# Kernel tuning notes

Measured on AMD Instinct MI355X. Metric: run time of the kernel, lower is better.

The kernel has to match this reference:

```python
import jax, jax.numpy as jnp
import numpy as np

N_NODES = 100000
N_EDGES = 1000000
IN_DIM = 128
HID1 = 64
HID2 = 64
OUT_DIM = 1
NUM_GRAPHS = 2048


def setup_inputs() -> dict:
    key = jax.random.key(0)
    ks = jax.random.split(key, 12)
    x = jax.random.normal(ks[0], (N_NODES, IN_DIM), dtype=jnp.float32)
    edge_index = jax.random.randint(ks[1], (2, N_EDGES), 0, N_NODES, dtype=jnp.int64)
    batch = jnp.sort(jax.random.randint(ks[2], (N_NODES,), 0, NUM_GRAPHS, dtype=jnp.int64))
    s1 = 1.0 / np.sqrt(IN_DIM)
    s2 = 1.0 / np.sqrt(HID1)
    s3 = 1.0 / np.sqrt(HID2)
    return {
        "x": x,
        "edge_index": edge_index,
        "batch": batch,
        "W1": jax.random.normal(ks[3], (IN_DIM, HID1), dtype=jnp.float32) * s1,
        "b1": jnp.zeros((HID1,), dtype=jnp.float32),
        "W2": jax.random.normal(ks[4], (HID1, HID2), dtype=jnp.float32) * s2,
        "b2": jnp.zeros((HID2,), dtype=jnp.float32),
        "attn_w": jax.random.normal(ks[5], (HID2, 1), dtype=jnp.float32) * s3,
        "attn_b": jnp.zeros((1,), dtype=jnp.float32),
        "mask_w": jax.random.normal(ks[6], (HID2, 1), dtype=jnp.float32) * s3,
        "mask_b": jnp.zeros((1,), dtype=jnp.float32),
        "out_w": jax.random.normal(ks[7], (HID2, OUT_DIM), dtype=jnp.float32) * s3,
        "out_b": jnp.zeros((OUT_DIM,), dtype=jnp.float32),
    }


def reference(x, edge_index, batch, W1, b1, W2, b2, attn_w, attn_b, mask_w, mask_b, out_w, out_b):
    n = x.shape[0]
    # GCNConv (PyG default): add self-loops, symmetric normalization
    loop = jnp.arange(n, dtype=edge_index.dtype)
    row = jnp.concatenate([edge_index[0], loop])  # source nodes
    col = jnp.concatenate([edge_index[1], loop])  # target nodes
    deg = jax.ops.segment_sum(jnp.ones_like(col, dtype=x.dtype), col, num_segments=n)
    dinv = jnp.where(deg > 0, jax.lax.rsqrt(jnp.maximum(deg, 1e-12)), 0.0)
    norm = dinv[row] * dinv[col]  # [E+N]

    def conv(h, W, b):
        h = h @ W                              # [N, out]
        m = h[row] * norm[:, None]             # gather + scale  [E+N, out]
        return jax.ops.segment_sum(m, col, num_segments=n) + b

    h = jax.nn.relu(conv(x, W1, b1))
    h = jax.nn.relu(conv(h, W2, b2))
    # AttentionPooling: (attn score * sigmoid mask)-weighted scatter-sum per graph
    scores = (h @ attn_w + attn_b) * jax.nn.sigmoid(h @ mask_w + mask_b)  # [N,1]
    pooled = jax.ops.segment_sum(h * scores, batch, num_segments=NUM_GRAPHS)  # [G, HID2]
    return pooled @ out_w + out_b
```

## Files before the change

kernel.cpp:

```cpp
#include <hip/hip_runtime.h>
#include <math.h>


#define NB 64
#define SEG 16
#define CAPS 80
#define SLOTS (SEG * CAPS)
#define BIN_BLOCKS 256

__global__ __launch_bounds__(256) void gemm_bin_kernel(
    const float* __restrict__ X, const float* __restrict__ W,
    float* __restrict__ P, int N, int K,
    const int* __restrict__ row, const int* __restrict__ col,
    int* __restrict__ bcnt, int* __restrict__ gbuf, int E,
    float* __restrict__ out, const float* __restrict__ out_b, int G) {
    __shared__ float Wl[32 * 64];
    __shared__ float xs[128 * 33];

    if (blockIdx.x < BIN_BLOCKS) {
        int seg = blockIdx.x & (SEG - 1);
        int t = blockIdx.x * 256 + threadIdx.x;
        if (t < G) out[t] = out_b[0];
        for (int e = t; e < E; e += BIN_BLOCKS * 256) {
            int c = col[e];
            int b = c >> 6;
            int pos = atomicAdd(&bcnt[(b * SEG + seg) * 16], 1);
            if (pos < CAPS) gbuf[b * SLOTS + seg * CAPS + pos] = row[e] | ((c & 63) << 17);
        }
        return;
    }

    const int tid = threadIdx.x;
    const int cg = tid & 3;
    const int ng = tid >> 2;
    const int node0 = (blockIdx.x - BIN_BLOCKS) * 128;

    float acc[2][16];
#pragma unroll
    for (int r = 0; r < 2; r++)
#pragma unroll
        for (int j = 0; j < 16; j++) acc[r][j] = 0.0f;

    for (int k0 = 0; k0 < K; k0 += 32) {
        const float4* Wg = (const float4*)(W + (size_t)k0 * 64);
#pragma unroll
        for (int f = tid; f < 512; f += 256) ((float4*)Wl)[f] = Wg[f];
        {
            int rrow = tid >> 1;
            int q0 = (tid & 1) * 16;
            int node = node0 + rrow;
            const float* Xr = X + (size_t)node * K + k0 + q0;
            float* xd = &xs[rrow * 33 + q0];
#pragma unroll
            for (int q = 0; q < 4; q++) {
                float4 v = make_float4(0.f, 0.f, 0.f, 0.f);
                if (node < N) v = *(const float4*)(Xr + 4 * q);
                xd[4 * q + 0] = v.x;
                xd[4 * q + 1] = v.y;
                xd[4 * q + 2] = v.z;
                xd[4 * q + 3] = v.w;
            }
        }
        __syncthreads();
#pragma unroll
        for (int kk = 0; kk < 32; kk++) {
            float xv0 = xs[(ng * 2 + 0) * 33 + kk];
            float xv1 = xs[(ng * 2 + 1) * 33 + kk];
            const float* wr = &Wl[kk * 64 + cg * 4];
            float4 w0 = *(const float4*)(wr + 0);
            float4 w1 = *(const float4*)(wr + 16);
            float4 w2 = *(const float4*)(wr + 32);
            float4 w3 = *(const float4*)(wr + 48);
#pragma unroll
            for (int r = 0; r < 2; r++) {
                float xv = r ? xv1 : xv0;
                acc[r][0]  = fmaf(xv, w0.x, acc[r][0]);
                acc[r][1]  = fmaf(xv, w0.y, acc[r][1]);
                acc[r][2]  = fmaf(xv, w0.z, acc[r][2]);
                acc[r][3]  = fmaf(xv, w0.w, acc[r][3]);
                acc[r][4]  = fmaf(xv, w1.x, acc[r][4]);
                acc[r][5]  = fmaf(xv, w1.y, acc[r][5]);
                acc[r][6]  = fmaf(xv, w1.z, acc[r][6]);
                acc[r][7]  = fmaf(xv, w1.w, acc[r][7]);
                acc[r][8]  = fmaf(xv, w2.x, acc[r][8]);
                acc[r][9]  = fmaf(xv, w2.y, acc[r][9]);
                acc[r][10] = fmaf(xv, w2.z, acc[r][10]);
                acc[r][11] = fmaf(xv, w2.w, acc[r][11]);
                acc[r][12] = fmaf(xv, w3.x, acc[r][12]);
                acc[r][13] = fmaf(xv, w3.y, acc[r][13]);
                acc[r][14] = fmaf(xv, w3.z, acc[r][14]);
                acc[r][15] = fmaf(xv, w3.w, acc[r][15]);
            }
        }
        __syncthreads();
    }

#pragma unroll
    for (int r = 0; r < 2; r++) {
        int node = node0 + ng * 2 + r;
        if (node < N) {
            float* dst = P + (size_t)node * 64 + cg * 4;
#pragma unroll
            for (int m = 0; m < 4; m++) {
                float4 v = make_float4(acc[r][4 * m + 0], acc[r][4 * m + 1],
                                       acc[r][4 * m + 2], acc[r][4 * m + 3]);
                *(float4*)(dst + 16 * m) = v;
            }
        }
    }
}

__global__ __launch_bounds__(256) void sort_scale_kernel(
    const int* __restrict__ bcnt, const int* __restrict__ gbuf,
    int* __restrict__ csr, int* __restrict__ startcnt,
    float* __restrict__ dinv, float* __restrict__ P, int N) {
    __shared__ int scnt[SEG], segoff[SEG], s_tot;
    __shared__ int ebuf[SLOTS];
    __shared__ int lcnt[NB], lstart[NB], lcur[NB];
    __shared__ float dinv_s[NB];
    const int tid = threadIdx.x;
    const int b = blockIdx.x;
    const int base = b * SLOTS;

    if (tid < SEG) {
        int c = bcnt[(b * SEG + tid) * 16];
        scnt[tid] = c < CAPS ? c : CAPS;
    }
    if (tid < NB) lcnt[tid] = 0;
    __syncthreads();
    if (tid == 0) {
        int o = 0;
        for (int s = 0; s < SEG; s++) { segoff[s] = o; o += scnt[s]; }
        s_tot = o;
    }
    __syncthreads();
    for (int idx = tid; idx < SLOTS; idx += 256) {
        int seg = idx / CAPS;
        int j = idx - seg * CAPS;
        if (j < scnt[seg]) {
            int w = gbuf[base + idx];
            ebuf[segoff[seg] + j] = w;
            atomicAdd(&lcnt[(w >> 17) & 63], 1);
        }
    }
    __syncthreads();
    if (tid < NB) {
        int cntv = lcnt[tid];
        int val = cntv;
#pragma unroll
        for (int off = 1; off < 64; off <<= 1) {
            int n = __shfl_up(val, off, 64);
            if (tid >= off) val += n;
        }
        int st = val - cntv;
        lstart[tid] = st;
        lcur[tid] = st;
        float dv = rsqrtf(1.0f + (float)cntv);
        dinv_s[tid] = dv;
        int v = b * NB + tid;
        if (v < N) {
            dinv[v] = dv;
            int cc = cntv < 127 ? cntv : 127;
            startcnt[v] = ((base + st) << 7) | cc;
        }
    }
    __syncthreads();
    int tot = s_tot;
    for (int idx = tid; idx < tot; idx += 256) {
        int w = ebuf[idx];
        int vl = (w >> 17) & 63;
        int pp = atomicAdd(&lcur[vl], 1);
        csr[base + pp] = w & 131071;
    }
    const int g = tid >> 4;
    const int p4 = (tid & 15) * 4;
    for (int s = 0; s < 4; s++) {
        int vl = g + s * 16;
        int v = b * NB + vl;
        if (v < N) {
            float d = dinv_s[vl];
            float4 x = *(const float4*)(P + (size_t)v * 64 + p4);
            x.x *= d; x.y *= d; x.z *= d; x.w *= d;
            *(float4*)(P + (size_t)v * 64 + p4) = x;
        }
    }
}

__global__ __launch_bounds__(256) void gather_kernel(
    const float* __restrict__ P, const int* __restrict__ csr,
    const int* __restrict__ startcnt, const float* __restrict__ dinv,
    const float* __restrict__ bias, float* __restrict__ B, int N) {
    int t = blockIdx.x * blockDim.x + threadIdx.x;
    int v = t >> 4;
    if (v >= N) return;
    int p4 = (t & 15) * 4;
    int pack = startcnt[v];
    int st = pack >> 7;
    int c = pack & 127;
    float dv = dinv[v];
    float4 acc = *(const float4*)(P + (size_t)v * 64 + p4);
    for (int i = 0; i < c; i += 4) {
        int i1 = (i + 1 < c) ? i + 1 : i;
        int i2 = (i + 2 < c) ? i + 2 : i;
        int i3 = (i + 3 < c) ? i + 3 : i;
        int u0 = csr[st + i], u1 = csr[st + i1], u2 = csr[st + i2], u3 = csr[st + i3];
        float4 m0 = *(const float4*)(P + (size_t)u0 * 64 + p4);
        float4 m1 = *(const float4*)(P + (size_t)u1 * 64 + p4);
        float4 m2 = *(const float4*)(P + (size_t)u2 * 64 + p4);
        float4 m3 = *(const float4*)(P + (size_t)u3 * 64 + p4);
        acc.x += m0.x; acc.y += m0.y; acc.z += m0.z; acc.w += m0.w;
        if (i + 1 < c) { acc.x += m1.x; acc.y += m1.y; acc.z += m1.z; acc.w += m1.w; }
        if (i + 2 < c) { acc.x += m2.x; acc.y += m2.y; acc.z += m2.z; acc.w += m2.w; }
        if (i + 3 < c) { acc.x += m3.x; acc.y += m3.y; acc.z += m3.z; acc.w += m3.w; }
    }
    float4 bb = *(const float4*)(bias + p4);
    float4 r;
    r.x = fmaxf(fmaf(acc.x, dv, bb.x), 0.f);
    r.y = fmaxf(fmaf(acc.y, dv, bb.y), 0.f);
    r.z = fmaxf(fmaf(acc.z, dv, bb.z), 0.f);
    r.w = fmaxf(fmaf(acc.w, dv, bb.w), 0.f);
    *(float4*)(B + (size_t)v * 64 + p4) = r;
}

__global__ __launch_bounds__(256) void gemm_scale_kernel(
    const float* __restrict__ X, const float* __restrict__ W,
    const float* __restrict__ dinv, float* __restrict__ Q, int N, int K) {
    __shared__ float Wl[32 * 64];
    __shared__ float xs[128 * 33];
    const int tid = threadIdx.x;
    const int cg = tid & 3;
    const int ng = tid >> 2;
    const int node0 = blockIdx.x * 128;

    float acc[2][16];
#pragma unroll
    for (int r = 0; r < 2; r++)
#pragma unroll
        for (int j = 0; j < 16; j++) acc[r][j] = 0.0f;

    for (int k0 = 0; k0 < K; k0 += 32) {
        const float4* Wg = (const float4*)(W + (size_t)k0 * 64);
#pragma unroll
        for (int f = tid; f < 512; f += 256) ((float4*)Wl)[f] = Wg[f];
        {
            int rrow = tid >> 1;
            int q0 = (tid & 1) * 16;
            int node = node0 + rrow;
            const float* Xr = X + (size_t)node * K + k0 + q0;
            float* xd = &xs[rrow * 33 + q0];
#pragma unroll
            for (int q = 0; q < 4; q++) {
                float4 v = make_float4(0.f, 0.f, 0.f, 0.f);
                if (node < N) v = *(const float4*)(Xr + 4 * q);
                xd[4 * q + 0] = v.x;
                xd[4 * q + 1] = v.y;
                xd[4 * q + 2] = v.z;
                xd[4 * q + 3] = v.w;
            }
        }
        __syncthreads();
#pragma unroll
        for (int kk = 0; kk < 32; kk++) {
            float xv0 = xs[(ng * 2 + 0) * 33 + kk];
            float xv1 = xs[(ng * 2 + 1) * 33 + kk];
            const float* wr = &Wl[kk * 64 + cg * 4];
            float4 w0 = *(const float4*)(wr + 0);
            float4 w1 = *(const float4*)(wr + 16);
            float4 w2 = *(const float4*)(wr + 32);
            float4 w3 = *(const float4*)(wr + 48);
#pragma unroll
            for (int r = 0; r < 2; r++) {
                float xv = r ? xv1 : xv0;
                acc[r][0]  = fmaf(xv, w0.x, acc[r][0]);
                acc[r][1]  = fmaf(xv, w0.y, acc[r][1]);
                acc[r][2]  = fmaf(xv, w0.z, acc[r][2]);
                acc[r][3]  = fmaf(xv, w0.w, acc[r][3]);
                acc[r][4]  = fmaf(xv, w1.x, acc[r][4]);
                acc[r][5]  = fmaf(xv, w1.y, acc[r][5]);
                acc[r][6]  = fmaf(xv, w1.z, acc[r][6]);
                acc[r][7]  = fmaf(xv, w1.w, acc[r][7]);
                acc[r][8]  = fmaf(xv, w2.x, acc[r][8]);
                acc[r][9]  = fmaf(xv, w2.y, acc[r][9]);
                acc[r][10] = fmaf(xv, w2.z, acc[r][10]);
                acc[r][11] = fmaf(xv, w2.w, acc[r][11]);
                acc[r][12] = fmaf(xv, w3.x, acc[r][12]);
                acc[r][13] = fmaf(xv, w3.y, acc[r][13]);
                acc[r][14] = fmaf(xv, w3.z, acc[r][14]);
                acc[r][15] = fmaf(xv, w3.w, acc[r][15]);
            }
        }
        __syncthreads();
    }

#pragma unroll
    for (int r = 0; r < 2; r++) {
        int node = node0 + ng * 2 + r;
        if (node < N) {
            float d = dinv[node];
            float* dst = Q + (size_t)node * 64 + cg * 4;
#pragma unroll
            for (int m = 0; m < 4; m++) {
                float4 v = make_float4(acc[r][4 * m + 0] * d, acc[r][4 * m + 1] * d,
                                       acc[r][4 * m + 2] * d, acc[r][4 * m + 3] * d);
                *(float4*)(dst + 16 * m) = v;
            }
        }
    }
}

#define GP_NODES 64
__global__ __launch_bounds__(256) void gather_pool_kernel(
    const float* __restrict__ Q, const int* __restrict__ csr,
    const int* __restrict__ startcnt, const float* __restrict__ dinv,
    const float* __restrict__ bias, const int* __restrict__ batch,
    const float* __restrict__ attn_w, const float* __restrict__ attn_b,
    const float* __restrict__ mask_w, const float* __restrict__ mask_b,
    const float* __restrict__ out_w, float* __restrict__ out, int N) {
    __shared__ float pacc[2048];
    __shared__ int s_gmin, s_span;
    const int tid = threadIdx.x;
    const int v0 = blockIdx.x * GP_NODES;
    const int vend = (v0 + GP_NODES < N) ? v0 + GP_NODES : N;
    if (tid == 0) {
        int gmin = batch[v0];
        s_gmin = gmin;
        s_span = batch[vend - 1] - gmin + 1;
    }
    __syncthreads();
    const int gmin = s_gmin, span = s_span;
    for (int i = tid; i < span; i += 256) pacc[i] = 0.f;
    __syncthreads();

    const int p = tid & 15;
    const int p4 = p * 4;
    const float4 wa = ((const float4*)attn_w)[p];
    const float4 wm = ((const float4*)mask_w)[p];
    const float4 wo = ((const float4*)out_w)[p];
    const float4 bb = ((const float4*)bias)[p];
    const float ab = attn_b[0], mb = mask_b[0];

    for (int v = v0 + (tid >> 4); v < vend; v += 16) {
        int pack = startcnt[v];
        int st = pack >> 7;
        int c = pack & 127;
        float dv = dinv[v];
        float4 acc = *(const float4*)(Q + (size_t)v * 64 + p4);
        for (int i = 0; i < c; i += 4) {
            int i1 = (i + 1 < c) ? i + 1 : i;
            int i2 = (i + 2 < c) ? i + 2 : i;
            int i3 = (i + 3 < c) ? i + 3 : i;
            int u0 = csr[st + i], u1 = csr[st + i1], u2 = csr[st + i2], u3 = csr[st + i3];
            float4 m0 = *(const float4*)(Q + (size_t)u0 * 64 + p4);
            float4 m1 = *(const float4*)(Q + (size_t)u1 * 64 + p4);
            float4 m2 = *(const float4*)(Q + (size_t)u2 * 64 + p4);
            float4 m3 = *(const float4*)(Q + (size_t)u3 * 64 + p4);
            acc.x += m0.x; acc.y += m0.y; acc.z += m0.z; acc.w += m0.w;
            if (i + 1 < c) { acc.x += m1.x; acc.y += m1.y; acc.z += m1.z; acc.w += m1.w; }
            if (i + 2 < c) { acc.x += m2.x; acc.y += m2.y; acc.z += m2.z; acc.w += m2.w; }
            if (i + 3 < c) { acc.x += m3.x; acc.y += m3.y; acc.z += m3.z; acc.w += m3.w; }
        }
        float hx = fmaxf(fmaf(acc.x, dv, bb.x), 0.f);
        float hy = fmaxf(fmaf(acc.y, dv, bb.y), 0.f);
        float hz = fmaxf(fmaf(acc.z, dv, bb.z), 0.f);
        float hw = fmaxf(fmaf(acc.w, dv, bb.w), 0.f);
        float pa = hx * wa.x + hy * wa.y + hz * wa.z + hw * wa.w;
        float pm = hx * wm.x + hy * wm.y + hz * wm.z + hw * wm.w;
        float po = hx * wo.x + hy * wo.y + hz * wo.z + hw * wo.w;
#pragma unroll
        for (int off = 1; off < 16; off <<= 1) {
            pa += __shfl_xor(pa, off, 64);
            pm += __shfl_xor(pm, off, 64);
            po += __shfl_xor(po, off, 64);
        }
        if (p == 0) {
            float cc = (pa + ab) * (1.0f / (1.0f + expf(-(pm + mb)))) * po;
            atomicAdd(&pacc[batch[v] - gmin], cc);
        }
    }
    __syncthreads();
    for (int i = tid; i < span; i += 256) {
        float val = pacc[i];
        if (val != 0.f) atomicAdd(&out[gmin + i], val);
    }
}

extern "C" void kernel_launch(void* const* d_in, const int* in_sizes, int n_in,
                              void* d_out, int out_size, void* d_ws, size_t ws_size,
                              hipStream_t stream) {
    const float* x      = (const float*)d_in[0];
    const int*   edge   = (const int*)d_in[1];
    const int*   batch  = (const int*)d_in[2];
    const float* W1     = (const float*)d_in[3];
    const float* b1     = (const float*)d_in[4];
    const float* W2     = (const float*)d_in[5];
    const float* b2     = (const float*)d_in[6];
    const float* attn_w = (const float*)d_in[7];
    const float* attn_b = (const float*)d_in[8];
    const float* mask_w = (const float*)d_in[9];
    const float* mask_b = (const float*)d_in[10];
    const float* out_w  = (const float*)d_in[11];
    const float* out_b  = (const float*)d_in[12];
    float* out = (float*)d_out;

    const int N  = in_sizes[2];
    const int E  = in_sizes[1] / 2;
    const int K1 = in_sizes[0] / N;
    const int H  = in_sizes[4];
    const int G  = out_size;
    const int* row = edge;
    const int* col = edge + E;

    const int NBUCK = (N + NB - 1) / NB;

    char* ws = (char*)d_ws;
    auto align256 = [](size_t s) { return (s + 255) / 256 * 256; };
    int*   bcnt     = (int*)ws;   ws += align256((size_t)NBUCK * SEG * 16 * 4);
    int*   gbuf     = (int*)ws;   ws += align256((size_t)NBUCK * SLOTS * 4);
    int*   csr      = (int*)ws;   ws += align256((size_t)NBUCK * SLOTS * 4);
    int*   startcnt = (int*)ws;   ws += align256((size_t)N * 4);
    float* dinv     = (float*)ws; ws += align256((size_t)N * 4);
    float* P        = (float*)ws; ws += align256((size_t)N * H * 4);
    float* B        = (float*)ws; ws += align256((size_t)N * H * 4);
    float* Q        = (float*)ws;

    const int gblocks = (N + 127) / 128;
    const int n16b = (N * 16 + 255) / 256;

    hipMemsetAsync(bcnt, 0, (size_t)NBUCK * SEG * 16 * 4, stream);

    gemm_bin_kernel<<<BIN_BLOCKS + gblocks, 256, 0, stream>>>(
        x, W1, P, N, K1, row, col, bcnt, gbuf, E, out, out_b, G);

    sort_scale_kernel<<<NBUCK, 256, 0, stream>>>(
        bcnt, gbuf, csr, startcnt, dinv, P, N);

    gather_kernel<<<n16b, 256, 0, stream>>>(P, csr, startcnt, dinv, b1, B, N);

    gemm_scale_kernel<<<gblocks, 256, 0, stream>>>(B, W2, dinv, Q, N, H);

    gather_pool_kernel<<<NBUCK, 256, 0, stream>>>(
        Q, csr, startcnt, dinv, b2, batch, attn_w, attn_b, mask_w, mask_b, out_w, out, N);
}
```

Measured before the change: 277.0 us.

## Drop P prescale pass, pad CSR rows to 4 and vectorize neighbor index loads

The sort kernel no longer rescales P by dinv. The first gather instead multiplies each neighbor row by that neighbor's dinv, fetched separately, which removes a full read-modify-write pass over P. CSR segments are padded to multiples of 4 and zeroed by a new memset, so both gather loops can load neighbor indices as int4 and process 8 neighbors per iteration. The cost is an extra memset of the CSR buffer and an extra dinv gather per edge in layer one. Padding also consumes more of the fixed per-bucket slots, which could overflow a bucket's capacity.

```diff
diff --git a/kernel.cpp b/kernel.cpp
--- a/kernel.cpp
+++ b/kernel.cpp
@@ -110,14 +110,13 @@
     }
 }
 
-__global__ __launch_bounds__(256) void sort_scale_kernel(
+__global__ __launch_bounds__(256) void sort_kernel(
     const int* __restrict__ bcnt, const int* __restrict__ gbuf,
     int* __restrict__ csr, int* __restrict__ startcnt,
-    float* __restrict__ dinv, float* __restrict__ P, int N) {
+    float* __restrict__ dinv, int N) {
     __shared__ int scnt[SEG], segoff[SEG], s_tot;
     __shared__ int ebuf[SLOTS];
-    __shared__ int lcnt[NB], lstart[NB], lcur[NB];
-    __shared__ float dinv_s[NB];
+    __shared__ int lcnt[NB], lcur[NB];
     const int tid = threadIdx.x;
     const int b = blockIdx.x;
     const int base = b * SLOTS;
@@ -146,20 +145,18 @@
     __syncthreads();
     if (tid < NB) {
         int cntv = lcnt[tid];
-        int val = cntv;
+        int rnd = (cntv + 3) & ~3;
+        int val = rnd;
 #pragma unroll
         for (int off = 1; off < 64; off <<= 1) {
             int n = __shfl_up(val, off, 64);
             if (tid >= off) val += n;
         }
-        int st = val - cntv;
-        lstart[tid] = st;
+        int st = val - rnd;
         lcur[tid] = st;
-        float dv = rsqrtf(1.0f + (float)cntv);
-        dinv_s[tid] = dv;
         int v = b * NB + tid;
         if (v < N) {
-            dinv[v] = dv;
+            dinv[v] = rsqrtf(1.0f + (float)cntv);
             int cc = cntv < 127 ? cntv : 127;
             startcnt[v] = ((base + st) << 7) | cc;
         }
@@ -171,18 +168,6 @@
         int vl = (w >> 17) & 63;
         int pp = atomicAdd(&lcur[vl], 1);
         csr[base + pp] = w & 131071;
-    }
-    const int g = tid >> 4;
-    const int p4 = (tid & 15) * 4;
-    for (int s = 0; s < 4; s++) {
-        int vl = g + s * 16;
-        int v = b * NB + vl;
-        if (v < N) {
-            float d = dinv_s[vl];
-            float4 x = *(const float4*)(P + (size_t)v * 64 + p4);
-            x.x *= d; x.y *= d; x.z *= d; x.w *= d;
-            *(float4*)(P + (size_t)v * 64 + p4) = x;
-        }
     }
 }
 
@@ -198,20 +183,37 @@
     int st = pack >> 7;
     int c = pack & 127;
     float dv = dinv[v];
-    float4 acc = *(const float4*)(P + (size_t)v * 64 + p4);
-    for (int i = 0; i < c; i += 4) {
-        int i1 = (i + 1 < c) ? i + 1 : i;
-        int i2 = (i + 2 < c) ? i + 2 : i;
-        int i3 = (i + 3 < c) ? i + 3 : i;
-        int u0 = csr[st + i], u1 = csr[st + i1], u2 = csr[st + i2], u3 = csr[st + i3];
-        float4 m0 = *(const float4*)(P + (size_t)u0 * 64 + p4);
-        float4 m1 = *(const float4*)(P + (size_t)u1 * 64 + p4);
-        float4 m2 = *(const float4*)(P + (size_t)u2 * 64 + p4);
-        float4 m3 = *(const float4*)(P + (size_t)u3 * 64 + p4);
-        acc.x += m0.x; acc.y += m0.y; acc.z += m0.z; acc.w += m0.w;
-        if (i + 1 < c) { acc.x += m1.x; acc.y += m1.y; acc.z += m1.z; acc.w += m1.w; }
-        if (i + 2 < c) { acc.x += m2.x; acc.y += m2.y; acc.z += m2.z; acc.w += m2.w; }
-        if (i + 3 < c) { acc.x += m3.x; acc.y += m3.y; acc.z += m3.z; acc.w += m3.w; }
+    float4 a0 = *(const float4*)(P + (size_t)v * 64 + p4);
+    float4 acc = make_float4(a0.x * dv, a0.y * dv, a0.z * dv, a0.w * dv);
+    for (int i = 0; i < c; i += 8) {
+        int4 ua = *(const int4*)(csr + st + i);
+        int4 ub = *(const int4*)(csr + st + i + 4);
+        float du0 = dinv[ua.x], du1 = dinv[ua.y], du2 = dinv[ua.z], du3 = dinv[ua.w];
+        float du4 = dinv[ub.x], du5 = dinv[ub.y], du6 = dinv[ub.z], du7 = dinv[ub.w];
+        float4 m0 = *(const float4*)(P + (size_t)ua.x * 64 + p4);
+        float4 m1 = *(const float4*)(P + (size_t)ua.y * 64 + p4);
+        float4 m2 = *(const float4*)(P + (size_t)ua.z * 64 + p4);
+        float4 m3 = *(const float4*)(P + (size_t)ua.w * 64 + p4);
+        float4 m4 = *(const float4*)(P + (size_t)ub.x * 64 + p4);
+        float4 m5 = *(const float4*)(P + (size_t)ub.y * 64 + p4);
+        float4 m6 = *(const float4*)(P + (size_t)ub.z * 64 + p4);
+        float4 m7 = *(const float4*)(P + (size_t)ub.w * 64 + p4);
+        acc.x = fmaf(m0.x, du0, acc.x); acc.y = fmaf(m0.y, du0, acc.y);
+        acc.z = fmaf(m0.z, du0, acc.z); acc.w = fmaf(m0.w, du0, acc.w);
+        if (i + 1 < c) { acc.x = fmaf(m1.x, du1, acc.x); acc.y = fmaf(m1.y, du1, acc.y);
+                         acc.z = fmaf(m1.z, du1, acc.z); acc.w = fmaf(m1.w, du1, acc.w); }
+        if (i + 2 < c) { acc.x = fmaf(m2.x, du2, acc.x); acc.y = fmaf(m2.y, du2, acc.y);
+                         acc.z = fmaf(m2.z, du2, acc.z); acc.w = fmaf(m2.w, du2, acc.w); }
+        if (i + 3 < c) { acc.x = fmaf(m3.x, du3, acc.x); acc.y = fmaf(m3.y, du3, acc.y);
+                         acc.z = fmaf(m3.z, du3, acc.z); acc.w = fmaf(m3.w, du3, acc.w); }
+        if (i + 4 < c) { acc.x = fmaf(m4.x, du4, acc.x); acc.y = fmaf(m4.y, du4, acc.y);
+                         acc.z = fmaf(m4.z, du4, acc.z); acc.w = fmaf(m4.w, du4, acc.w); }
+        if (i + 5 < c) { acc.x = fmaf(m5.x, du5, acc.x); acc.y = fmaf(m5.y, du5, acc.y);
+                         acc.z = fmaf(m5.z, du5, acc.z); acc.w = fmaf(m5.w, du5, acc.w); }
+        if (i + 6 < c) { acc.x = fmaf(m6.x, du6, acc.x); acc.y = fmaf(m6.y, du6, acc.y);
+                         acc.z = fmaf(m6.z, du6, acc.z); acc.w = fmaf(m6.w, du6, acc.w); }
+        if (i + 7 < c) { acc.x = fmaf(m7.x, du7, acc.x); acc.y = fmaf(m7.y, du7, acc.y);
+                         acc.z = fmaf(m7.z, du7, acc.z); acc.w = fmaf(m7.w, du7, acc.w); }
     }
     float4 bb = *(const float4*)(bias + p4);
     float4 r;
@@ -345,19 +347,25 @@
         int c = pack & 127;
         float dv = dinv[v];
         float4 acc = *(const float4*)(Q + (size_t)v * 64 + p4);
-        for (int i = 0; i < c; i += 4) {
-            int i1 = (i + 1 < c) ? i + 1 : i;
-            int i2 = (i + 2 < c) ? i + 2 : i;
-            int i3 = (i + 3 < c) ? i + 3 : i;
-            int u0 = csr[st + i], u1 = csr[st + i1], u2 = csr[st + i2], u3 = csr[st + i3];
-            float4 m0 = *(const float4*)(Q + (size_t)u0 * 64 + p4);
-            float4 m1 = *(const float4*)(Q + (size_t)u1 * 64 + p4);
-            float4 m2 = *(const float4*)(Q + (size_t)u2 * 64 + p4);
-            float4 m3 = *(const float4*)(Q + (size_t)u3 * 64 + p4);
+        for (int i = 0; i < c; i += 8) {
+            int4 ua = *(const int4*)(csr + st + i);
+            int4 ub = *(const int4*)(csr + st + i + 4);
+            float4 m0 = *(const float4*)(Q + (size_t)ua.x * 64 + p4);
+            float4 m1 = *(const float4*)(Q + (size_t)ua.y * 64 + p4);
+            float4 m2 = *(const float4*)(Q + (size_t)ua.z * 64 + p4);
+            float4 m3 = *(const float4*)(Q + (size_t)ua.w * 64 + p4);
+            float4 m4 = *(const float4*)(Q + (size_t)ub.x * 64 + p4);
+            float4 m5 = *(const float4*)(Q + (size_t)ub.y * 64 + p4);
+            float4 m6 = *(const float4*)(Q + (size_t)ub.z * 64 + p4);
+            float4 m7 = *(const float4*)(Q + (size_t)ub.w * 64 + p4);
             acc.x += m0.x; acc.y += m0.y; acc.z += m0.z; acc.w += m0.w;
             if (i + 1 < c) { acc.x += m1.x; acc.y += m1.y; acc.z += m1.z; acc.w += m1.w; }
             if (i + 2 < c) { acc.x += m2.x; acc.y += m2.y; acc.z += m2.z; acc.w += m2.w; }
             if (i + 3 < c) { acc.x += m3.x; acc.y += m3.y; acc.z += m3.z; acc.w += m3.w; }
+            if (i + 4 < c) { acc.x += m4.x; acc.y += m4.y; acc.z += m4.z; acc.w += m4.w; }
+            if (i + 5 < c) { acc.x += m5.x; acc.y += m5.y; acc.z += m5.z; acc.w += m5.w; }
+            if (i + 6 < c) { acc.x += m6.x; acc.y += m6.y; acc.z += m6.z; acc.w += m6.w; }
+            if (i + 7 < c) { acc.x += m7.x; acc.y += m7.y; acc.z += m7.z; acc.w += m7.w; }
         }
         float hx = fmaxf(fmaf(acc.x, dv, bb.x), 0.f);
         float hy = fmaxf(fmaf(acc.y, dv, bb.y), 0.f);
@@ -427,12 +435,12 @@
     const int n16b = (N * 16 + 255) / 256;
 
     hipMemsetAsync(bcnt, 0, (size_t)NBUCK * SEG * 16 * 4, stream);
+    hipMemsetAsync(csr, 0, (size_t)NBUCK * SLOTS * 4, stream);
 
     gemm_bin_kernel<<<BIN_BLOCKS + gblocks, 256, 0, stream>>>(
         x, W1, P, N, K1, row, col, bcnt, gbuf, E, out, out_b, G);
 
-    sort_scale_kernel<<<NBUCK, 256, 0, stream>>>(
-        bcnt, gbuf, csr, startcnt, dinv, P, N);
+    sort_kernel<<<NBUCK, 256, 0, stream>>>(bcnt, gbuf, csr, startcnt, dinv, N);
 
     gather_kernel<<<n16b, 256, 0, stream>>>(P, csr, startcnt, dinv, b1, B, N);
 
```

Measured after the change: 282.0 us. No clear change (+1.8%).
